# Performance work log

Measured on AMD Instinct MI355X. Metric: run time of the kernel, lower is better.

## Reference

```python
import jax, jax.numpy as jnp
import numpy as np

DIM = 512
NH = 16
HEAD = DIM // NH  # 32
WS1 = 8   # window_size // 2 (shift_h=True)
WS2 = 16  # window_size
SHIFT = 4  # window_size // 4


def _rotary(t, cos, sin):
    # t: (..., C); split even/odd channels, rotate, concat halves
    x1, x2 = t[..., 0::2], t[..., 1::2]
    return jnp.concatenate([x1 * cos - x2 * sin, x2 * cos + x1 * sin], axis=-1)


def setup_inputs() -> dict:
    key = jax.random.key(0)
    ks = jax.random.split(key, 8)
    B, H, W = 8, 64, 64
    G = (H // WS1) * (W // WS2)  # 32
    N = WS1 * WS2                # 128
    s = 1.0 / np.sqrt(DIM)
    return {
        "x": jax.random.normal(ks[0], (B, H, W, DIM), jnp.float32),
        "pos_embed_q": jax.random.normal(ks[1], (2, G, 1, N, HEAD // 2), jnp.float32),
        "pos_embed_kv": jax.random.normal(ks[2], (2, G, 1, 2 * N, HEAD // 2), jnp.float32),
        "mask": jnp.zeros((G, 1, N, 2 * N), jnp.float32),
        "w_q": jax.random.normal(ks[3], (DIM, DIM), jnp.float32) * s,
        "b_q": jnp.zeros((DIM,), jnp.float32),
        "w_kv": jax.random.normal(ks[4], (DIM, 2 * DIM), jnp.float32) * s,
        "b_kv": jnp.zeros((2 * DIM,), jnp.float32),
        "w_proj": jax.random.normal(ks[5], (DIM, DIM), jnp.float32) * s,
        "b_proj": jnp.zeros((DIM,), jnp.float32),
        "H": H,
        "W": W,
    }


def reference(x, pos_embed_q, pos_embed_kv, mask, w_q, b_q, w_kv, b_kv, w_proj, b_proj, H, W):
    B = x.shape[0]
    G = (H // WS1) * (W // WS2)
    N = WS1 * WS2
    C = HEAD

    # q projection + window partition -> (B, G, nH, N, C)
    q = x @ w_q + b_q
    q = q.reshape(B, H // WS1, WS1, W // WS2, WS2, NH, C)
    q = q.transpose(0, 1, 3, 5, 2, 4, 6).reshape(B, G, NH, N, C)

    # kv projection, two opposite rolls along H, window partition -> (2, B, G, nH, 2N, C)
    kv = x @ w_kv + b_kv                              # (B,H,W,2D)
    kvs = jnp.stack([jnp.roll(kv, -SHIFT, axis=1), jnp.roll(kv, SHIFT, axis=1)])  # (2shift,B,H,W,2D)
    kvs = kvs.reshape(2, B, H // WS1, WS1, W // WS2, WS2, 2, NH, C)
    kvs = kvs.transpose(6, 1, 2, 4, 7, 0, 3, 5, 8).reshape(2, B, G, NH, 2 * N, C)
    k, v = kvs[0], kvs[1]

    # rotary position embedding
    q = _rotary(q, pos_embed_q[0], pos_embed_q[1])
    k = _rotary(k, pos_embed_kv[0], pos_embed_kv[1])

    # scaled dot product attention with additive mask (eval: no dropout)
    scale = 1.0 / np.sqrt(C)
    scores = jnp.einsum('bgnqc,bgnkc->bgnqk', q, k) * scale + mask
    attn = jax.nn.softmax(scores, axis=-1)
    o = jnp.einsum('bgnqk,bgnkc->bgnqc', attn, v)     # (B,G,nH,N,C)

    # window un-partition -> (B, H, W, D), output projection
    o = o.reshape(B, H // WS1, W // WS2, NH, WS1, WS2, C)
    o = o.transpose(0, 1, 4, 2, 5, 3, 6).reshape(B, H, W, DIM)
    return o @ w_proj + b_proj
```

## Files before the change

kernel.cpp:

```cpp
#include <hip/hip_runtime.h>

typedef __bf16 bf16x8 __attribute__((ext_vector_type(8)));
typedef __bf16 bf16x4 __attribute__((ext_vector_type(4)));
typedef float f32x4 __attribute__((ext_vector_type(4)));

#define DEV __device__ __forceinline__

DEV f32x4 mfma16(bf16x8 a, bf16x8 b, f32x4 c) {
    return __builtin_amdgcn_mfma_f32_16x16x32_bf16(a, b, c, 0, 0, 0);
}

DEV void async16(const void* g, void* l) {
    __builtin_amdgcn_global_load_lds((__attribute__((address_space(1))) void*)g,
                                     (__attribute__((address_space(3))) void*)l, 16, 0, 0);
}

#define LDS_FENCE() asm volatile("" ::: "memory")
#define BARRIER() asm volatile("s_barrier" ::: "memory")
#define VMCNT(n) asm volatile("s_waitcnt vmcnt(" #n ")" ::: "memory")

__global__ __launch_bounds__(256) void cast_x_kernel(const float4* __restrict__ in,
                                                     bf16x8* __restrict__ out) {
    int i = blockIdx.x * 256 + threadIdx.x;
    float4 a = in[2 * i], b = in[2 * i + 1];
    bf16x8 o;
    o[0] = (__bf16)a.x; o[1] = (__bf16)a.y; o[2] = (__bf16)a.z; o[3] = (__bf16)a.w;
    o[4] = (__bf16)b.x; o[5] = (__bf16)b.y; o[6] = (__bf16)b.z; o[7] = (__bf16)b.w;
    out[i] = o;
}

__global__ void transpose_cast_kernel(const float* __restrict__ src,
                                      __bf16* __restrict__ dst, int R, int C) {
    __shared__ float tile[32][33];
    int tx = threadIdx.x, ty = threadIdx.y;
    int c0 = blockIdx.x * 32, r0 = blockIdx.y * 32;
#pragma unroll
    for (int j = 0; j < 4; ++j)
        tile[ty + j * 8][tx] = src[(size_t)(r0 + ty + j * 8) * C + c0 + tx];
    __syncthreads();
#pragma unroll
    for (int j = 0; j < 4; ++j)
        dst[(size_t)(c0 + ty + j * 8) * R + r0 + tx] = (__bf16)tile[tx][ty + j * 8];
}

__global__ __launch_bounds__(256) void mask_flag_kernel(const float* __restrict__ mask,
                                                        int* __restrict__ flags) {
    int g = blockIdx.x;
    const float4* m4 = (const float4*)(mask + (size_t)g * 32768);
    int any = 0;
    for (int i = threadIdx.x; i < 8192; i += 256) {
        float4 v = m4[i];
        any |= (v.x != 0.f) | (v.y != 0.f) | (v.z != 0.f) | (v.w != 0.f);
    }
    any = __any(any) ? 1 : 0;
    __shared__ int s;
    if (threadIdx.x == 0) s = 0;
    __syncthreads();
    if ((threadIdx.x & 63) == 0 && any) atomicOr(&s, 1);
    __syncthreads();
    if (threadIdx.x == 0) flags[g] = s;
}

__global__ __launch_bounds__(512, 2) void gemm256(const __bf16* __restrict__ A,
                                                  const __bf16* __restrict__ Bt,
                                                  const float* __restrict__ bias0,
                                                  const float* __restrict__ bias1,
                                                  void* __restrict__ Cout, int N, int mode) {
    __shared__ __bf16 As[2][256 * 64];
    __shared__ __bf16 Bs[2][256 * 64];
    const int tid = threadIdx.x;
    const int bm = blockIdx.x, bn = blockIdx.y;
    const int lane = tid & 63, wv = tid >> 6;
    const int quad = lane >> 4, l16 = lane & 15;
    const int wm = (wv >> 2) * 128, wn = (wv & 3) * 64;
    const __bf16* Abase = A + (size_t)bm * 256 * 512;
    const __bf16* Bbase = Bt + (size_t)bn * 256 * 512;

    int s_off[4];
#pragma unroll
    for (int i = 0; i < 4; ++i) {
        int chunk = i * 512 + tid;
        int r = chunk >> 3, cc = chunk & 7;
        s_off[i] = r * 512 + ((cc ^ (r & 7)) << 3);
    }

    f32x4 acc[8][4] = {};

#pragma unroll
    for (int i = 0; i < 4; ++i) {
        int chunk = i * 512 + tid;
        async16(Abase + s_off[i], &As[0][chunk * 8]);
        async16(Bbase + s_off[i], &Bs[0][chunk * 8]);
    }

    for (int kt = 0; kt < 8; ++kt) {
        const int c = kt & 1;
        if (kt < 7) {
#pragma unroll
            for (int i = 0; i < 4; ++i) {
                int chunk = i * 512 + tid;
                async16(Abase + s_off[i] + (kt + 1) * 64, &As[c ^ 1][chunk * 8]);
                async16(Bbase + s_off[i] + (kt + 1) * 64, &Bs[c ^ 1][chunk * 8]);
            }
            VMCNT(8);
        } else {
            VMCNT(0);
        }
        BARRIER();

        const __bf16* Ab = &As[c][0];
        const __bf16* Bb = &Bs[c][0];
#pragma unroll
        for (int ks = 0; ks < 2; ++ks) {
            bf16x8 af[8], bfm[4];
            const int cch = ks * 4 + quad;
#pragma unroll
            for (int t = 0; t < 8; ++t) {
                int ra = wm + t * 16 + l16;
                af[t] = *(const bf16x8*)&Ab[ra * 64 + ((cch ^ (ra & 7)) << 3)];
            }
#pragma unroll
            for (int t = 0; t < 4; ++t) {
                int rb = wn + t * 16 + l16;
                bfm[t] = *(const bf16x8*)&Bb[rb * 64 + ((cch ^ (rb & 7)) << 3)];
            }
            __builtin_amdgcn_s_setprio(1);
#pragma unroll
            for (int mt = 0; mt < 8; ++mt)
#pragma unroll
                for (int nt = 0; nt < 4; ++nt)
                    acc[mt][nt] = mfma16(af[mt], bfm[nt], acc[mt][nt]);
            __builtin_amdgcn_s_setprio(0);
            BARRIER();
        }
    }

#pragma unroll
    for (int nt = 0; nt < 4; ++nt) {
        int ng = bn * 256 + wn + nt * 16 + l16;
        float bias = (ng < 512) ? bias0[ng] : bias1[ng - 512];
        if (mode == 0) {
            int type = ng >> 9, nhh = (ng >> 5) & 15, ch = ng & 31;
            __bf16* dst = (__bf16*)Cout + (size_t)type * 16777216 + (size_t)nhh * 1048576 + ch;
#pragma unroll
            for (int mt = 0; mt < 8; ++mt)
#pragma unroll
                for (int r = 0; r < 4; ++r) {
                    int mg = bm * 256 + wm + mt * 16 + quad * 4 + r;
                    dst[(size_t)mg * 32] = (__bf16)(acc[mt][nt][r] + bias);
                }
        } else {
#pragma unroll
            for (int mt = 0; mt < 8; ++mt)
#pragma unroll
                for (int r = 0; r < 4; ++r) {
                    int mg = bm * 256 + wm + mt * 16 + quad * 4 + r;
                    ((float*)Cout)[(size_t)mg * N + ng] = acc[mt][nt][r] + bias;
                }
        }
    }
}

#define ATT_SCALE 0.17677669529663687f

__global__ __launch_bounds__(256, 4) void attn_kernel(const __bf16* __restrict__ qkv,
                                                      const float* __restrict__ peq,
                                                      const float* __restrict__ pekv,
                                                      const float* __restrict__ mask,
                                                      const int* __restrict__ mflags,
                                                      __bf16* __restrict__ oatt) {
    __shared__ __align__(16) char smem[38400];
    __bf16* Ks = (__bf16*)smem;
    __bf16* Vt = (__bf16*)(smem + 16384);
    __bf16* Ps = (__bf16*)(smem + 33280);

    const int tid = threadIdx.x;
    const int bid = ((blockIdx.x & 7) << 9) | (blockIdx.x >> 3);
    const int b = bid >> 9;
    const int g = (bid >> 4) & 31;
    const int nh = bid & 15;
    const int gh = g >> 2, gw = g & 3;
    const int lane = tid & 63, wv = tid >> 6;
    const int quad = lane >> 4, l16 = lane & 15;

    const __bf16* qq = qkv + (size_t)nh * 1048576;
    const __bf16* kkp = qkv + 16777216 + (size_t)nh * 1048576;
    const __bf16* vvp = qkv + 33554432 + (size_t)nh * 1048576;

#pragma unroll
    for (int it = 0; it < 4; ++it) {
        int item = it * 256 + tid;
        int ko = item >> 2, c8 = item & 3;
        int roll = ko >> 7, n = ko & 127;
        int h = (gh * 8 + (n >> 4) + (roll ? 60 : 4)) & 63;
        int w = gw * 16 + (n & 15);
        int row = (b * 64 + h) * 64 + w;
        bf16x8 v = *(const bf16x8*)(kkp + (size_t)row * 32 + c8 * 8);
        int pidx = (g * 256 + ko) * 16 + c8 * 4;
        float4 c4 = *(const float4*)(pekv + pidx);
        float4 s4 = *(const float4*)(pekv + 131072 + pidx);
        float cs[4] = {c4.x, c4.y, c4.z, c4.w}, sn[4] = {s4.x, s4.y, s4.z, s4.w};
        bf16x4 lo, hi;
#pragma unroll
        for (int j = 0; j < 4; ++j) {
            float k0 = (float)v[2 * j], k1 = (float)v[2 * j + 1];
            lo[j] = (__bf16)(k0 * cs[j] - k1 * sn[j]);
            hi[j] = (__bf16)(k1 * cs[j] + k0 * sn[j]);
        }
        int sw = (ko >> 1) & 3;
        int base = ko * 32, off = (c8 & 1) * 4;
        *(bf16x4*)&Ks[base + (((c8 >> 1) ^ sw) << 3) + off]       = lo;
        *(bf16x4*)&Ks[base + (((2 + (c8 >> 1)) ^ sw) << 3) + off] = hi;
    }
#pragma unroll
    for (int it = 0; it < 4; ++it) {
        int ko = tid;
        int roll = ko >> 7, n = ko & 127;
        int h = (gh * 8 + (n >> 4) + (roll ? 60 : 4)) & 63;
        int w = gw * 16 + (n & 15);
        int row = (b * 64 + h) * 64 + w;
        bf16x8 v = *(const bf16x8*)(vvp + (size_t)row * 32 + it * 8);
#pragma unroll
        for (int j = 0; j < 8; ++j)
            Vt[(it * 8 + j) * 264 + ko] = v[j];
    }

    bf16x8 aq[2];
    {
        const int halfsel = quad & 1;
        const bool hi_half = quad >= 2;
#pragma unroll
        for (int rt = 0; rt < 2; ++rt) {
            int n = wv * 32 + rt * 16 + l16;
            int h = gh * 8 + (n >> 4), w = gw * 16 + (n & 15);
            int row = (b * 64 + h) * 64 + w;
            const __bf16* qp = qq + (size_t)row * 32 + halfsel * 16;
            bf16x8 rA = *(const bf16x8*)qp;
            bf16x8 rB = *(const bf16x8*)(qp + 8);
            int pb = (g * 128 + n) * 16 + halfsel * 8;
            float4 ca = *(const float4*)(peq + pb);
            float4 cb = *(const float4*)(peq + pb + 4);
            float4 sa = *(const float4*)(peq + 65536 + pb);
            float4 sb = *(const float4*)(peq + 65536 + pb + 4);
            float cc[8] = {ca.x, ca.y, ca.z, ca.w, cb.x, cb.y, cb.z, cb.w};
            float ss[8] = {sa.x, sa.y, sa.z, sa.w, sb.x, sb.y, sb.z, sb.w};
#pragma unroll
            for (int j = 0; j < 8; ++j) {
                float q0 = (float)(j < 4 ? rA[2 * j] : rB[2 * (j - 4)]);
                float q1 = (float)(j < 4 ? rA[2 * j + 1] : rB[2 * (j - 4) + 1]);
                float r = hi_half ? (q1 * cc[j] + q0 * ss[j]) : (q0 * cc[j] - q1 * ss[j]);
                aq[rt][j] = (__bf16)(r * ATT_SCALE);
            }
        }
    }
    __syncthreads();

    f32x4 o00 = {}, o01 = {}, o10 = {}, o11 = {};
    f32x4 rs0 = {}, rs1 = {};
    const bool use_mask = mflags[g] != 0;
    const float* mg = mask + (size_t)g * 32768;
    __bf16* Pw = Ps + wv * 640;
    const int arow = l16 * 40 + quad * 8;

#pragma unroll 2
    for (int ch = 0; ch < 8; ++ch) {
        bf16x8 vb0 = *(const bf16x8*)&Vt[l16 * 264 + ch * 32 + quad * 8];
        bf16x8 vb1 = *(const bf16x8*)&Vt[(16 + l16) * 264 + ch * 32 + quad * 8];
        f32x4 z = {0.f, 0.f, 0.f, 0.f};
        int key0 = ch * 32 + l16, key1 = key0 + 16;
        bf16x8 bk0 = *(const bf16x8*)&Ks[key0 * 32 + ((quad ^ ((key0 >> 1) & 3)) << 3)];
        bf16x8 bk1 = *(const bf16x8*)&Ks[key1 * 32 + ((quad ^ ((key1 >> 1) & 3)) << 3)];
        f32x4 s00 = mfma16(aq[0], bk0, z), s01 = mfma16(aq[0], bk1, z);
        f32x4 s10 = mfma16(aq[1], bk0, z), s11 = mfma16(aq[1], bk1, z);

        if (use_mask) {
#pragma unroll
            for (int r = 0; r < 4; ++r) {
                int r0 = (wv * 32 + quad * 4 + r) * 256 + ch * 32 + l16;
                int r1 = (wv * 32 + 16 + quad * 4 + r) * 256 + ch * 32 + l16;
                s00[r] += mg[r0];      s01[r] += mg[r0 + 16];
                s10[r] += mg[r1];      s11[r] += mg[r1 + 16];
            }
        }
#pragma unroll
        for (int r = 0; r < 4; ++r) {
            s00[r] = __expf(s00[r]); s01[r] = __expf(s01[r]);
            s10[r] = __expf(s10[r]); s11[r] = __expf(s11[r]);
            rs0[r] += s00[r] + s01[r];
            rs1[r] += s10[r] + s11[r];
        }
#pragma unroll
        for (int r = 0; r < 4; ++r) {
            Pw[(quad * 4 + r) * 40 + l16]      = (__bf16)s00[r];
            Pw[(quad * 4 + r) * 40 + 16 + l16] = (__bf16)s01[r];
        }
        LDS_FENCE();
        bf16x8 a0 = *(const bf16x8*)&Pw[arow];
        LDS_FENCE();
#pragma unroll
        for (int r = 0; r < 4; ++r) {
            Pw[(quad * 4 + r) * 40 + l16]      = (__bf16)s10[r];
            Pw[(quad * 4 + r) * 40 + 16 + l16] = (__bf16)s11[r];
        }
        LDS_FENCE();
        bf16x8 a1 = *(const bf16x8*)&Pw[arow];
        LDS_FENCE();
        o00 = mfma16(a0, vb0, o00); o01 = mfma16(a0, vb1, o01);
        o10 = mfma16(a1, vb0, o10); o11 = mfma16(a1, vb1, o11);
    }

#pragma unroll
    for (int off = 1; off < 16; off <<= 1) {
#pragma unroll
        for (int r = 0; r < 4; ++r) {
            rs0[r] += __shfl_xor(rs0[r], off);
            rs1[r] += __shfl_xor(rs1[r], off);
        }
    }
#pragma unroll
    for (int r = 0; r < 4; ++r) { rs0[r] = 1.f / rs0[r]; rs1[r] = 1.f / rs1[r]; }

#pragma unroll
    for (int r = 0; r < 4; ++r) {
        {
            int rown = wv * 32 + quad * 4 + r;
            int h = gh * 8 + (rown >> 4), w = gw * 16 + (rown & 15);
            size_t base = ((size_t)(b * 64 + h) * 64 + w) * 512 + nh * 32;
            oatt[base + l16]      = (__bf16)(o00[r] * rs0[r]);
            oatt[base + 16 + l16] = (__bf16)(o01[r] * rs0[r]);
        }
        {
            int rown = wv * 32 + 16 + quad * 4 + r;
            int h = gh * 8 + (rown >> 4), w = gw * 16 + (rown & 15);
            size_t base = ((size_t)(b * 64 + h) * 64 + w) * 512 + nh * 32;
            oatt[base + l16]      = (__bf16)(o10[r] * rs1[r]);
            oatt[base + 16 + l16] = (__bf16)(o11[r] * rs1[r]);
        }
    }
}

extern "C" void kernel_launch(void* const* d_in, const int* in_sizes, int n_in,
                              void* d_out, int out_size, void* d_ws, size_t ws_size,
                              hipStream_t stream) {
    const float* x     = (const float*)d_in[0];
    const float* peq   = (const float*)d_in[1];
    const float* pekv  = (const float*)d_in[2];
    const float* mask  = (const float*)d_in[3];
    const float* wq    = (const float*)d_in[4];
    const float* bq    = (const float*)d_in[5];
    const float* wkv   = (const float*)d_in[6];
    const float* bkv   = (const float*)d_in[7];
    const float* wproj = (const float*)d_in[8];
    const float* bproj = (const float*)d_in[9];
    float* out = (float*)d_out;

    char* ws = (char*)d_ws;
    __bf16* xb    = (__bf16*)(ws);
    __bf16* oatt  = (__bf16*)(ws);
    __bf16* wqkvT = (__bf16*)(ws + 33554432);
    int*    mflag = (int*)(ws + 33554432);
    __bf16* wpT   = (__bf16*)(ws + 35127296);
    __bf16* qkv   = (__bf16*)(ws + 35651584);

    cast_x_kernel<<<8192, 256, 0, stream>>>((const float4*)x, (bf16x8*)xb);
    transpose_cast_kernel<<<dim3(16, 16), dim3(32, 8), 0, stream>>>(wq, wqkvT, 512, 512);
    transpose_cast_kernel<<<dim3(32, 16), dim3(32, 8), 0, stream>>>(wkv, wqkvT + 512 * 512, 512, 1024);
    transpose_cast_kernel<<<dim3(16, 16), dim3(32, 8), 0, stream>>>(wproj, wpT, 512, 512);

    gemm256<<<dim3(128, 6), 512, 0, stream>>>(xb, wqkvT, bq, bkv, qkv, 1536, 0);
    mask_flag_kernel<<<32, 256, 0, stream>>>(mask, mflag);
    attn_kernel<<<4096, 256, 0, stream>>>(qkv, peq, pekv, mask, mflag, oatt);
    gemm256<<<dim3(128, 2), 512, 0, stream>>>(oatt, wpT, bproj, bproj, out, 512, 1);
}
```

Before: 317.6 us.

## Split GEMM K-tiles into half units with finer-grained staged prefetch

Restructures the 256x256 GEMM mainloop so each 64-wide K tile is stored as two 32-wide half units, with a new XOR swizzle for the narrower rows. Loads are issued one unit per phase, interleaved with four MFMA phases per K step, and run up to two K steps ahead. The aim is to overlap global-to-LDS traffic with compute more smoothly and cut stall time at the barriers. In exchange there are more barriers per K step and more intricate vmcnt bookkeeping, which could race or serialize if the counts are wrong.

```diff
diff --git a/kernel.cpp b/kernel.cpp
--- a/kernel.cpp
+++ b/kernel.cpp
@@ -61,13 +61,23 @@
     if (threadIdx.x == 0) flags[g] = s;
 }
 
+DEV void stage_unit(const __bf16* __restrict__ Gbase, __bf16* unit, int tid, int koff) {
+#pragma unroll
+    for (int i = 0; i < 2; ++i) {
+        int d = i * 512 + tid;
+        int r = d >> 2;
+        int cc = (d & 3) ^ ((r >> 2) & 3);
+        async16(Gbase + (size_t)r * 512 + koff + cc * 8, unit + d * 8);
+    }
+}
+
 __global__ __launch_bounds__(512, 2) void gemm256(const __bf16* __restrict__ A,
                                                   const __bf16* __restrict__ Bt,
                                                   const float* __restrict__ bias0,
                                                   const float* __restrict__ bias1,
                                                   void* __restrict__ Cout, int N, int mode) {
-    __shared__ __bf16 As[2][256 * 64];
-    __shared__ __bf16 Bs[2][256 * 64];
+    __shared__ __bf16 As[2][2][256 * 32];
+    __shared__ __bf16 Bs[2][2][256 * 32];
     const int tid = threadIdx.x;
     const int bm = blockIdx.x, bn = blockIdx.y;
     const int lane = tid & 63, wv = tid >> 6;
@@ -76,61 +86,51 @@
     const __bf16* Abase = A + (size_t)bm * 256 * 512;
     const __bf16* Bbase = Bt + (size_t)bn * 256 * 512;
 
-    int s_off[4];
-#pragma unroll
-    for (int i = 0; i < 4; ++i) {
-        int chunk = i * 512 + tid;
-        int r = chunk >> 3, cc = chunk & 7;
-        s_off[i] = r * 512 + ((cc ^ (r & 7)) << 3);
-    }
-
     f32x4 acc[8][4] = {};
 
-#pragma unroll
-    for (int i = 0; i < 4; ++i) {
-        int chunk = i * 512 + tid;
-        async16(Abase + s_off[i], &As[0][chunk * 8]);
-        async16(Bbase + s_off[i], &Bs[0][chunk * 8]);
-    }
-
+    stage_unit(Abase, &As[0][0][0], tid, 0 * 64 + 0);
+    stage_unit(Bbase, &Bs[0][0][0], tid, 0 * 64 + 0);
+    stage_unit(Abase, &As[0][1][0], tid, 0 * 64 + 32);
+    stage_unit(Bbase, &Bs[0][1][0], tid, 0 * 64 + 32);
+    stage_unit(Abase, &As[1][0][0], tid, 1 * 64 + 0);
+    stage_unit(Bbase, &Bs[1][0][0], tid, 1 * 64 + 0);
+    VMCNT(8);
+    BARRIER();
+
+#pragma unroll
     for (int kt = 0; kt < 8; ++kt) {
-        const int c = kt & 1;
-        if (kt < 7) {
-#pragma unroll
-            for (int i = 0; i < 4; ++i) {
-                int chunk = i * 512 + tid;
-                async16(Abase + s_off[i] + (kt + 1) * 64, &As[c ^ 1][chunk * 8]);
-                async16(Bbase + s_off[i] + (kt + 1) * 64, &Bs[c ^ 1][chunk * 8]);
+        const int par = kt & 1;
+        bf16x8 bfm[4];
+#pragma unroll
+        for (int ph = 0; ph < 4; ++ph) {
+            const int mh = ph & 1, ks = ph >> 1;
+            bf16x8 af[4];
+            if (mh == 0) {
+#pragma unroll
+                for (int t = 0; t < 4; ++t) {
+                    int rb = wn + t * 16 + l16;
+                    bfm[t] = *(const bf16x8*)&Bs[par][ks][rb * 32 + ((quad ^ ((rb >> 2) & 3)) << 3)];
+                }
             }
-            VMCNT(8);
-        } else {
-            VMCNT(0);
-        }
-        BARRIER();
-
-        const __bf16* Ab = &As[c][0];
-        const __bf16* Bb = &Bs[c][0];
-#pragma unroll
-        for (int ks = 0; ks < 2; ++ks) {
-            bf16x8 af[8], bfm[4];
-            const int cch = ks * 4 + quad;
-#pragma unroll
-            for (int t = 0; t < 8; ++t) {
-                int ra = wm + t * 16 + l16;
-                af[t] = *(const bf16x8*)&Ab[ra * 64 + ((cch ^ (ra & 7)) << 3)];
+#pragma unroll
+            for (int t = 0; t < 4; ++t) {
+                int ra = wm + mh * 64 + t * 16 + l16;
+                af[t] = *(const bf16x8*)&As[par][ks][ra * 32 + ((quad ^ ((ra >> 2) & 3)) << 3)];
             }
-#pragma unroll
-            for (int t = 0; t < 4; ++t) {
-                int rb = wn + t * 16 + l16;
-                bfm[t] = *(const bf16x8*)&Bb[rb * 64 + ((cch ^ (rb & 7)) << 3)];
-            }
+            if (ph == 0 && kt + 1 < 8) stage_unit(Abase, &As[par ^ 1][1][0], tid, (kt + 1) * 64 + 32);
+            if (ph == 1 && kt + 1 < 8) stage_unit(Bbase, &Bs[par ^ 1][1][0], tid, (kt + 1) * 64 + 32);
+            if (ph == 2 && kt + 2 < 8) stage_unit(Abase, &As[par][0][0], tid, (kt + 2) * 64 + 0);
+            if (ph == 3 && kt + 2 < 8) stage_unit(Bbase, &Bs[par][0][0], tid, (kt + 2) * 64 + 0);
+            BARRIER();
             __builtin_amdgcn_s_setprio(1);
 #pragma unroll
-            for (int mt = 0; mt < 8; ++mt)
+            for (int mt = 0; mt < 4; ++mt)
 #pragma unroll
                 for (int nt = 0; nt < 4; ++nt)
-                    acc[mt][nt] = mfma16(af[mt], bfm[nt], acc[mt][nt]);
+                    acc[mh * 4 + mt][nt] = mfma16(af[mt], bfm[nt], acc[mh * 4 + mt][nt]);
             __builtin_amdgcn_s_setprio(0);
+            if (ph == 1) { if (kt < 7) { VMCNT(8); } else { VMCNT(0); } }
+            if (ph == 3) { if (kt < 6) { VMCNT(8); } else if (kt == 6) { VMCNT(4); } }
             BARRIER();
         }
     }
@@ -146,7 +146,7 @@
             for (int mt = 0; mt < 8; ++mt)
 #pragma unroll
                 for (int r = 0; r < 4; ++r) {
-                    int mg = bm * 256 + wm + mt * 16 + quad * 4 + r;
+                    int mg = bm * 256 + wm + (mt >> 2) * 64 + (mt & 3) * 16 + quad * 4 + r;
                     dst[(size_t)mg * 32] = (__bf16)(acc[mt][nt][r] + bias);
                 }
         } else {
@@ -154,7 +154,7 @@
             for (int mt = 0; mt < 8; ++mt)
 #pragma unroll
                 for (int r = 0; r < 4; ++r) {
-                    int mg = bm * 256 + wm + mt * 16 + quad * 4 + r;
+                    int mg = bm * 256 + wm + (mt >> 2) * 64 + (mt & 3) * 16 + quad * 4 + r;
                     ((float*)Cout)[(size_t)mg * N + ng] = acc[mt][nt][r] + bias;
                 }
         }
```

Result: slower. 328.8 us (+3.5%).
